# Performance work log

Hardware: AMD Instinct MI355X
Metric: run time of the kernel (lower is better)

The kernel has to match this reference:

```python
import jax, jax.numpy as jnp
import numpy as np

N = 50000   # nodes
E = 500000  # edges
F = 256     # node feature dim
ED = 64     # edge feature dim
H = 128     # hidden channels
O = 32      # out channels
NEG_SLOPE = 0.2
EPS = 1e-16


def setup_inputs() -> dict:
    key = jax.random.key(0)
    ks = jax.random.split(key, 16)
    s = 0.05
    return {
        "x": jax.random.normal(ks[0], (N, F), jnp.float32),
        "edge_index": jax.random.randint(ks[1], (2, E), 0, N, dtype=jnp.int32),
        "edge_attr": jax.random.normal(ks[2], (E, ED), jnp.float32),
        # layer 1 (embed): F -> H
        "W1": jax.random.normal(ks[3], (F, H), jnp.float32) * s,
        "att_src1": jax.random.normal(ks[4], (H,), jnp.float32) * s,
        "att_dst1": jax.random.normal(ks[5], (H,), jnp.float32) * s,
        "We1": jax.random.normal(ks[6], (ED, H), jnp.float32) * s,
        "att_edge1": jax.random.normal(ks[7], (H,), jnp.float32) * s,
        "b1": jnp.zeros((H,), jnp.float32),
        # layer 2 (classifier): H -> O
        "W2": jax.random.normal(ks[8], (H, O), jnp.float32) * s,
        "att_src2": jax.random.normal(ks[9], (O,), jnp.float32) * s,
        "att_dst2": jax.random.normal(ks[10], (O,), jnp.float32) * s,
        "We2": jax.random.normal(ks[11], (ED, O), jnp.float32) * s,
        "att_edge2": jax.random.normal(ks[12], (O,), jnp.float32) * s,
        "b2": jnp.zeros((O,), jnp.float32),
    }


def _add_self_loops_mean(src, dst, ea, n):
    # PyG add_self_loops(fill_value='mean'): self-loop edge_attr = mean of
    # incoming edge_attr per target node (0 for isolated nodes).
    ones = jnp.ones((ea.shape[0],), ea.dtype)
    cnt = jax.ops.segment_sum(ones, dst, num_segments=n)
    summ = jax.ops.segment_sum(ea, dst, num_segments=n)  # [n, ED]
    mean = summ / jnp.maximum(cnt, 1.0)[:, None]
    loop = jnp.arange(n, dtype=src.dtype)
    return (jnp.concatenate([src, loop]),
            jnp.concatenate([dst, loop]),
            jnp.concatenate([ea, mean], axis=0))


def _gat_conv(x, src, dst, ea, W, a_src, a_dst, We, a_edge, b):
    n = x.shape[0]
    src, dst, ea = _add_self_loops_mean(src, dst, ea, n)
    h = x @ W                       # [n, C]
    he = ea @ We                    # [E', C]
    a_s = h @ a_src                 # [n]
    a_d = h @ a_dst                 # [n]
    a_e = he @ a_edge               # [E']
    alpha = a_s[src] + a_d[dst] + a_e
    alpha = jax.nn.leaky_relu(alpha, NEG_SLOPE)
    # segment softmax over incoming edges of each target node
    m = jax.ops.segment_max(alpha, dst, num_segments=n)
    ex = jnp.exp(alpha - m[dst])
    denom = jax.ops.segment_sum(ex, dst, num_segments=n)
    coef = ex / (denom[dst] + EPS)
    out = jax.ops.segment_sum(coef[:, None] * h[src], dst, num_segments=n)
    return out + b


def reference(x, edge_index, edge_attr,
              W1, att_src1, att_dst1, We1, att_edge1, b1,
              W2, att_src2, att_dst2, We2, att_edge2, b2):
    src, dst = edge_index[0], edge_index[1]
    x1 = _gat_conv(x, src, dst, edge_attr, W1, att_src1, att_dst1, We1, att_edge1, b1)
    h = jax.nn.relu(x1)  # Dropout(0.5) is identity in eval mode
    out = _gat_conv(h, src, dst, edge_attr, W2, att_src2, att_dst2, We2, att_edge2, b2)
    return (out, h)
```

## Files before the change

kernel.cpp:

```cpp
#include <hip/hip_runtime.h>

#define N_NODES 50000
#define N_EDGES 500000
#define F_DIM 256
#define ED_DIM 64
#define H_DIM 128
#define O_DIM 32
#define NEG_SLOPE 0.2f
#define EPS_F 1e-16f

#define GB1 391
#define EDGE_BLOCKS 4096

typedef __attribute__((ext_vector_type(8))) short short8;
typedef __attribute__((ext_vector_type(4))) float floatx4;

__device__ __forceinline__ unsigned short f2bf(float f) {
    union { float f; unsigned u; } c; c.f = f;
    unsigned u = c.u;
    return (unsigned short)((u + 0x7fffu + ((u >> 16) & 1u)) >> 16);
}
__device__ __forceinline__ float leaky(float a) { return a > 0.f ? a : a * NEG_SLOPE; }

__global__ void k_prep(const float* __restrict__ We1, const float* __restrict__ aev1,
                       const float* __restrict__ We2, const float* __restrict__ aev2,
                       float* __restrict__ wv1, float* __restrict__ wv2,
                       const float* __restrict__ W1, const float* __restrict__ W2,
                       unsigned short* __restrict__ W1T, unsigned short* __restrict__ W2T) {
    if (blockIdx.x == 32) {
        int t = threadIdx.x;
        if (t < 64) {
            float s = 0.f;
            for (int c = 0; c < H_DIM; c++) s += We1[t * H_DIM + c] * aev1[c];
            wv1[t] = s;
        } else if (t < 128) {
            int k = t - 64;
            float s = 0.f;
            for (int c = 0; c < O_DIM; c++) s += We2[k * O_DIM + c] * aev2[c];
            wv2[k] = s;
        }
        return;
    }
    int gid = blockIdx.x * 256 + threadIdx.x;
    const int stride = 32 * 256;
    for (int i = gid; i < H_DIM * F_DIM; i += stride) {
        int n = i >> 8, k = i & 255;
        W1T[i] = f2bf(W1[k * H_DIM + n]);
    }
    for (int i = gid; i < O_DIM * H_DIM; i += stride) {
        int n = i >> 7, k = i & 127;
        W2T[i] = f2bf(W2[k * O_DIM + n]);
    }
}

__global__ __launch_bounds__(256) void k_fused1(
        const float* __restrict__ A, const unsigned short* __restrict__ BT,
        const float* __restrict__ asv, const float* __restrict__ adv,
        float* __restrict__ C, float* __restrict__ a_s, float* __restrict__ a_d,
        const float* __restrict__ ea, const int* __restrict__ dst,
        const float* __restrict__ wv1, const float* __restrict__ wv2,
        float2* __restrict__ ae12, int* __restrict__ cnt) {
    __shared__ unsigned short As[128 * 40];
    __shared__ unsigned short Bs[128 * 40];
    int tid = threadIdx.x;
    int wave = tid >> 6, lane = tid & 63;

    if (blockIdx.x >= GB1) {
        int bid = blockIdx.x - GB1;
        int sub = lane & 15, eo = lane >> 4;
        float4 w1 = ((const float4*)wv1)[sub];
        float4 w2 = ((const float4*)wv2)[sub];
        int e0 = (bid * 4 + wave) * 4 + eo;
        const int stride = EDGE_BLOCKS * 16;
        for (int e = e0; e < N_EDGES; e += stride) {
            float4 q = *(const float4*)(ea + (size_t)e * ED_DIM + sub * 4);
            float s1 = q.x * w1.x + q.y * w1.y + q.z * w1.z + q.w * w1.w;
            float s2 = q.x * w2.x + q.y * w2.y + q.z * w2.z + q.w * w2.w;
#pragma unroll
            for (int o = 1; o < 16; o <<= 1) {
                s1 += __shfl_xor(s1, o);
                s2 += __shfl_xor(s2, o);
            }
            if (sub == 0) {
                ae12[e] = make_float2(s1, s2);
                atomicAdd(&cnt[dst[e]], 1);
            }
        }
        return;
    }

    int q = lane >> 4, r = lane & 15;
    int bm0 = blockIdx.x * 128;
    floatx4 acc[2][8];
#pragma unroll
    for (int a = 0; a < 2; a++)
#pragma unroll
        for (int b = 0; b < 8; b++) acc[a][b] = (floatx4){0.f, 0.f, 0.f, 0.f};

    int rr = tid >> 3;
    int kc = tid & 7;
    for (int k0 = 0; k0 < 256; k0 += 32) {
#pragma unroll
        for (int i = 0; i < 4; i++) {
            int row = rr + 32 * i;
            int gr = bm0 + row;
            float4 v = make_float4(0.f, 0.f, 0.f, 0.f);
            if (gr < N_NODES) v = *(const float4*)(A + (size_t)gr * 256 + k0 + kc * 4);
            unsigned lo = (unsigned)f2bf(v.x) | ((unsigned)f2bf(v.y) << 16);
            unsigned hi = (unsigned)f2bf(v.z) | ((unsigned)f2bf(v.w) << 16);
            *(uint2*)&As[row * 40 + kc * 4] = make_uint2(lo, hi);
        }
#pragma unroll
        for (int i = 0; i < 2; i++) {
            int idx = tid + 256 * i;
            int n = idx >> 2, ck = idx & 3;
            *(uint4*)&Bs[n * 40 + ck * 8] = *(const uint4*)(BT + n * 256 + k0 + ck * 8);
        }
        __syncthreads();
        short8 af[2], bf[8];
#pragma unroll
        for (int rt = 0; rt < 2; rt++)
            af[rt] = *(const short8*)&As[(wave * 32 + rt * 16 + r) * 40 + q * 8];
#pragma unroll
        for (int nt = 0; nt < 8; nt++)
            bf[nt] = *(const short8*)&Bs[(nt * 16 + r) * 40 + q * 8];
#pragma unroll
        for (int rt = 0; rt < 2; rt++)
#pragma unroll
            for (int nt = 0; nt < 8; nt++)
                acc[rt][nt] = __builtin_amdgcn_mfma_f32_16x16x32_bf16(af[rt], bf[nt], acc[rt][nt], 0, 0, 0);
        __syncthreads();
    }
#pragma unroll
    for (int rt = 0; rt < 2; rt++) {
        int rowb = bm0 + wave * 32 + rt * 16 + q * 4;
        float ps[4] = {0.f, 0.f, 0.f, 0.f}, pd[4] = {0.f, 0.f, 0.f, 0.f};
#pragma unroll
        for (int nt = 0; nt < 8; nt++) {
            int col = nt * 16 + r;
            float av = asv[col], dv = adv[col];
#pragma unroll
            for (int reg = 0; reg < 4; reg++) {
                float v = acc[rt][nt][reg];
                if (rowb + reg < N_NODES) C[(size_t)(rowb + reg) * 128 + col] = v;
                ps[reg] += v * av;
                pd[reg] += v * dv;
            }
        }
#pragma unroll
        for (int reg = 0; reg < 4; reg++) {
#pragma unroll
            for (int off = 1; off < 16; off <<= 1) {
                ps[reg] += __shfl_xor(ps[reg], off);
                pd[reg] += __shfl_xor(pd[reg], off);
            }
        }
        if (r == 0) {
#pragma unroll
            for (int reg = 0; reg < 4; reg++) {
                if (rowb + reg < N_NODES) { a_s[rowb + reg] = ps[reg]; a_d[rowb + reg] = pd[reg]; }
            }
        }
    }
}

__global__ void k_scan1(const int* __restrict__ cnt, int* __restrict__ bsum, int n) {
    __shared__ int sh[256];
    int b = blockIdx.x, t = threadIdx.x;
    int base = b * 1024;
    int s = 0;
    for (int j = 0; j < 4; j++) {
        int idx = base + t * 4 + j;
        if (idx < n) s += cnt[idx];
    }
    sh[t] = s; __syncthreads();
    for (int o = 128; o > 0; o >>= 1) {
        if (t < o) sh[t] += sh[t + o];
        __syncthreads();
    }
    if (t == 0) bsum[b] = sh[0];
}

__global__ void k_scan2(const int* __restrict__ bsum, int* __restrict__ bpre,
                        int* __restrict__ offs, int nb, int n) {
    if (threadIdx.x == 0) {
        int run = 0;
        for (int b = 0; b < nb; b++) { bpre[b] = run; run += bsum[b]; }
        offs[n] = run;
    }
}

__global__ void k_scan3(const int* __restrict__ cnt, const int* __restrict__ bpre,
                        int* __restrict__ offs, int* __restrict__ cursor, int n) {
    __shared__ int sh[256];
    int b = blockIdx.x, t = threadIdx.x;
    int base = b * 1024;
    int v[4]; int s = 0;
    for (int j = 0; j < 4; j++) {
        int idx = base + t * 4 + j;
        v[j] = (idx < n) ? cnt[idx] : 0;
        s += v[j];
    }
    sh[t] = s; __syncthreads();
    for (int o = 1; o < 256; o <<= 1) {
        int x = (t >= o) ? sh[t - o] : 0;
        __syncthreads();
        sh[t] += x;
        __syncthreads();
    }
    int texcl = sh[t] - s + bpre[b];
    int run = 0;
    for (int j = 0; j < 4; j++) {
        int idx = base + t * 4 + j;
        if (idx < n) { offs[idx] = texcl + run; cursor[idx] = texcl + run; }
        run += v[j];
    }
}

__global__ __launch_bounds__(256) void k_scatter(const int* __restrict__ src, const int* __restrict__ dst,
                          const float2* __restrict__ ae12, const float* __restrict__ a_s1,
                          int* __restrict__ cursor, float4* __restrict__ csr) {
    int e = blockIdx.x * blockDim.x + threadIdx.x;
    if (e >= N_EDGES) return;
    int s = src[e];
    int d = dst[e];
    float2 a = ae12[e];
    float as = a_s1[s];
    int p = atomicAdd(&cursor[d], 1);
    csr[p] = make_float4(__int_as_float(s), a.x, a.y, as);
}

template <bool RELU>
__global__ __launch_bounds__(256) void k_agg128(const float* __restrict__ h,
                         const float* __restrict__ a_s, const float* __restrict__ a_d,
                         const int* __restrict__ offs, const float4* __restrict__ csr,
                         const float* __restrict__ bias,
                         float* __restrict__ out) {
    int wave = threadIdx.x >> 6, lane = threadIdx.x & 63;
    int i = blockIdx.x * 4 + wave;
    int r = lane & 15;
    int g = lane >> 4;
    int rs = offs[i], re = offs[i + 1];
    int deg = re - rs;
    float adl = a_d[i];
    float4 acc0 = {0.f, 0.f, 0.f, 0.f}, acc1 = {0.f, 0.f, 0.f, 0.f};
    float dsum = 0.f, sum_ae = 0.f;
    for (int base = rs; base < re; base += 64) {
        int el = base + lane;
        float ex = 0.f, aev = 0.f; int s = 0;
        if (el < re) {
            float4 c = csr[el];
            s = __float_as_int(c.x);
            aev = c.y;
            ex = __expf(leaky(c.w + adl + aev));
        }
        dsum += ex; sum_ae += aev;
        int nv = (re - base) < 64 ? (re - base) : 64;
        int kmax = (nv + 3) >> 2;
        for (int k = 0; k < kmax; k++) {
            int t = g + 4 * k;
            float ext = __shfl(ex, t);
            int st = __shfl(s, t);
            if (t < nv) {
                const float4* hr = (const float4*)(h + (size_t)st * 128);
                float4 v0 = hr[r * 2], v1 = hr[r * 2 + 1];
                acc0.x += ext * v0.x; acc0.y += ext * v0.y; acc0.z += ext * v0.z; acc0.w += ext * v0.w;
                acc1.x += ext * v1.x; acc1.y += ext * v1.y; acc1.z += ext * v1.z; acc1.w += ext * v1.w;
            }
        }
    }
#pragma unroll
    for (int o = 32; o > 0; o >>= 1) {
        dsum += __shfl_xor(dsum, o);
        sum_ae += __shfl_xor(sum_ae, o);
    }
    float loop_ae = sum_ae / (float)(deg > 1 ? deg : 1);
    float al = leaky(a_s[i] + adl + loop_ae);
    float exs = __expf(al);
    float* a0 = (float*)&acc0; float* a1 = (float*)&acc1;
#pragma unroll
    for (int c = 0; c < 4; c++) {
        a0[c] += __shfl_xor(a0[c], 16); a0[c] += __shfl_xor(a0[c], 32);
        a1[c] += __shfl_xor(a1[c], 16); a1[c] += __shfl_xor(a1[c], 32);
    }
    if (g == 0) {
        float inv = 1.0f / (dsum + exs + EPS_F);
        const float4* hr = (const float4*)(h + (size_t)i * 128);
        float4 h0 = hr[r * 2], h1 = hr[r * 2 + 1];
        const float4* bp = (const float4*)bias;
        float4 b0 = bp[r * 2], b1 = bp[r * 2 + 1];
        float4 o0, o1;
        o0.x = (a0[0] + exs * h0.x) * inv + b0.x;
        o0.y = (a0[1] + exs * h0.y) * inv + b0.y;
        o0.z = (a0[2] + exs * h0.z) * inv + b0.z;
        o0.w = (a0[3] + exs * h0.w) * inv + b0.w;
        o1.x = (a1[0] + exs * h1.x) * inv + b1.x;
        o1.y = (a1[1] + exs * h1.y) * inv + b1.y;
        o1.z = (a1[2] + exs * h1.z) * inv + b1.z;
        o1.w = (a1[3] + exs * h1.w) * inv + b1.w;
        if (RELU) {
            o0.x = fmaxf(o0.x, 0.f); o0.y = fmaxf(o0.y, 0.f); o0.z = fmaxf(o0.z, 0.f); o0.w = fmaxf(o0.w, 0.f);
            o1.x = fmaxf(o1.x, 0.f); o1.y = fmaxf(o1.y, 0.f); o1.z = fmaxf(o1.z, 0.f); o1.w = fmaxf(o1.w, 0.f);
        }
        float4* op = (float4*)(out + (size_t)i * 128);
        op[r * 2] = o0;
        op[r * 2 + 1] = o1;
    }
}

__global__ __launch_bounds__(256) void k_gemm2(const float* __restrict__ A,
        const unsigned short* __restrict__ BT,
        const float* __restrict__ asv, const float* __restrict__ adv,
        float* __restrict__ C, float* __restrict__ a_s, float* __restrict__ a_d, int M) {
    __shared__ unsigned short As[128 * 40];
    __shared__ unsigned short Bs[32 * 40];
    int tid = threadIdx.x;
    int wave = tid >> 6, lane = tid & 63;
    int q = lane >> 4, r = lane & 15;
    int bm0 = blockIdx.x * 128;
    floatx4 acc[2][2];
#pragma unroll
    for (int a = 0; a < 2; a++)
#pragma unroll
        for (int b = 0; b < 2; b++) acc[a][b] = (floatx4){0.f, 0.f, 0.f, 0.f};

    int rr = tid >> 3;
    int kc = tid & 7;
    for (int k0 = 0; k0 < 128; k0 += 32) {
#pragma unroll
        for (int i = 0; i < 4; i++) {
            int row = rr + 32 * i;
            int gr = bm0 + row;
            float4 v = make_float4(0.f, 0.f, 0.f, 0.f);
            if (gr < M) v = *(const float4*)(A + (size_t)gr * 128 + k0 + kc * 4);
            unsigned lo = (unsigned)f2bf(v.x) | ((unsigned)f2bf(v.y) << 16);
            unsigned hi = (unsigned)f2bf(v.z) | ((unsigned)f2bf(v.w) << 16);
            *(uint2*)&As[row * 40 + kc * 4] = make_uint2(lo, hi);
        }
        if (tid < 128) {
            int n = tid >> 2, ck = tid & 3;
            *(uint4*)&Bs[n * 40 + ck * 8] = *(const uint4*)(BT + n * 128 + k0 + ck * 8);
        }
        __syncthreads();
        short8 af[2], bf[2];
#pragma unroll
        for (int rt = 0; rt < 2; rt++)
            af[rt] = *(const short8*)&As[(wave * 32 + rt * 16 + r) * 40 + q * 8];
#pragma unroll
        for (int nt = 0; nt < 2; nt++)
            bf[nt] = *(const short8*)&Bs[(nt * 16 + r) * 40 + q * 8];
#pragma unroll
        for (int rt = 0; rt < 2; rt++)
#pragma unroll
            for (int nt = 0; nt < 2; nt++)
                acc[rt][nt] = __builtin_amdgcn_mfma_f32_16x16x32_bf16(af[rt], bf[nt], acc[rt][nt], 0, 0, 0);
        __syncthreads();
    }
#pragma unroll
    for (int rt = 0; rt < 2; rt++) {
        int rowb = bm0 + wave * 32 + rt * 16 + q * 4;
        float ps[4] = {0.f, 0.f, 0.f, 0.f}, pd[4] = {0.f, 0.f, 0.f, 0.f};
#pragma unroll
        for (int nt = 0; nt < 2; nt++) {
            int col = nt * 16 + r;
            float av = asv[col], dv = adv[col];
#pragma unroll
            for (int reg = 0; reg < 4; reg++) {
                float v = acc[rt][nt][reg];
                if (rowb + reg < M) C[(size_t)(rowb + reg) * 32 + col] = v;
                ps[reg] += v * av;
                pd[reg] += v * dv;
            }
        }
#pragma unroll
        for (int reg = 0; reg < 4; reg++) {
#pragma unroll
            for (int off = 1; off < 16; off <<= 1) {
                ps[reg] += __shfl_xor(ps[reg], off);
                pd[reg] += __shfl_xor(pd[reg], off);
            }
        }
        if (r == 0) {
#pragma unroll
            for (int reg = 0; reg < 4; reg++) {
                if (rowb + reg < M) { a_s[rowb + reg] = ps[reg]; a_d[rowb + reg] = pd[reg]; }
            }
        }
    }
}

__global__ __launch_bounds__(256) void k_agg32(const float* __restrict__ h,
                        const float* __restrict__ a_s, const float* __restrict__ a_d,
                        const int* __restrict__ offs, const float4* __restrict__ csr,
                        const float* __restrict__ bias,
                        float* __restrict__ out) {
    int wave = threadIdx.x >> 6, lane = threadIdx.x & 63;
    int i = blockIdx.x * 4 + wave;
    int r = lane & 7;
    int g = lane >> 3;
    int rs = offs[i], re = offs[i + 1];
    int deg = re - rs;
    float adl = a_d[i];
    float4 acc = {0.f, 0.f, 0.f, 0.f};
    float dsum = 0.f, sum_ae = 0.f;
    for (int base = rs; base < re; base += 64) {
        int el = base + lane;
        float ex = 0.f, aev = 0.f; int s = 0;
        if (el < re) {
            float4 c = csr[el];
            s = __float_as_int(c.x);
            aev = c.z;
            ex = __expf(leaky(a_s[s] + adl + aev));
        }
        dsum += ex; sum_ae += aev;
        int nv = (re - base) < 64 ? (re - base) : 64;
        int kmax = (nv + 7) >> 3;
        for (int k = 0; k < kmax; k++) {
            int t = g + 8 * k;
            float ext = __shfl(ex, t);
            int st = __shfl(s, t);
            if (t < nv) {
                float4 v = ((const float4*)(h + (size_t)st * 32))[r];
                acc.x += ext * v.x; acc.y += ext * v.y; acc.z += ext * v.z; acc.w += ext * v.w;
            }
        }
    }
#pragma unroll
    for (int o = 32; o > 0; o >>= 1) {
        dsum += __shfl_xor(dsum, o);
        sum_ae += __shfl_xor(sum_ae, o);
    }
    float loop_ae = sum_ae / (float)(deg > 1 ? deg : 1);
    float al = leaky(a_s[i] + adl + loop_ae);
    float exs = __expf(al);
#pragma unroll
    for (int o = 8; o < 64; o <<= 1) {
        acc.x += __shfl_xor(acc.x, o); acc.y += __shfl_xor(acc.y, o);
        acc.z += __shfl_xor(acc.z, o); acc.w += __shfl_xor(acc.w, o);
    }
    if (g == 0) {
        float inv = 1.0f / (dsum + exs + EPS_F);
        float4 hv = ((const float4*)(h + (size_t)i * 32))[r];
        float4 bv = ((const float4*)bias)[r];
        float4 ov;
        ov.x = (acc.x + exs * hv.x) * inv + bv.x;
        ov.y = (acc.y + exs * hv.y) * inv + bv.y;
        ov.z = (acc.z + exs * hv.z) * inv + bv.z;
        ov.w = (acc.w + exs * hv.w) * inv + bv.w;
        ((float4*)(out + (size_t)i * 32))[r] = ov;
    }
}

extern "C" void kernel_launch(void* const* d_in, const int* in_sizes, int n_in,
                              void* d_out, int out_size, void* d_ws, size_t ws_size,
                              hipStream_t stream) {
    const float* x    = (const float*)d_in[0];
    const int* ei     = (const int*)d_in[1];
    const float* ea   = (const float*)d_in[2];
    const float* W1   = (const float*)d_in[3];
    const float* as1v = (const float*)d_in[4];
    const float* ad1v = (const float*)d_in[5];
    const float* We1  = (const float*)d_in[6];
    const float* aev1 = (const float*)d_in[7];
    const float* b1   = (const float*)d_in[8];
    const float* W2   = (const float*)d_in[9];
    const float* as2v = (const float*)d_in[10];
    const float* ad2v = (const float*)d_in[11];
    const float* We2  = (const float*)d_in[12];
    const float* aev2 = (const float*)d_in[13];
    const float* b2   = (const float*)d_in[14];

    const int* src = ei;
    const int* dst = ei + N_EDGES;

    char* w = (char*)d_ws;
    size_t off = 0;
    auto alloc = [&](size_t bytes) -> void* {
        void* p = w + off;
        off += bytes;
        off = (off + 255) & ~(size_t)255;
        return p;
    };
    float* h1      = (float*)alloc((size_t)N_NODES * H_DIM * 4);
    float* h2      = (float*)alloc((size_t)N_NODES * O_DIM * 4);
    float2* ae12   = (float2*)alloc((size_t)N_EDGES * 8);
    int* cnt       = (int*)alloc((size_t)N_NODES * 4);
    int* offs      = (int*)alloc((size_t)(N_NODES + 1) * 4);
    int* cursor    = (int*)alloc((size_t)N_NODES * 4);
    float4* csr    = (float4*)alloc((size_t)N_EDGES * 16);
    int* bsum      = (int*)alloc(64 * 4);
    int* bpre      = (int*)alloc(64 * 4);
    float* wv1     = (float*)alloc(64 * 4);
    float* wv2     = (float*)alloc(64 * 4);
    float* a_s1    = (float*)alloc((size_t)N_NODES * 4);
    float* a_d1    = (float*)alloc((size_t)N_NODES * 4);
    float* a_s2    = (float*)alloc((size_t)N_NODES * 4);
    float* a_d2    = (float*)alloc((size_t)N_NODES * 4);
    unsigned short* W1T = (unsigned short*)alloc((size_t)H_DIM * F_DIM * 2);
    unsigned short* W2T = (unsigned short*)alloc((size_t)O_DIM * H_DIM * 2);

    hipMemsetAsync(cnt, 0, (size_t)N_NODES * 4, stream);

    k_prep<<<33, 256, 0, stream>>>(We1, aev1, We2, aev2, wv1, wv2, W1, W2, W1T, W2T);

    k_fused1<<<GB1 + EDGE_BLOCKS, 256, 0, stream>>>(x, W1T, as1v, ad1v,
                                                    h1, a_s1, a_d1,
                                                    ea, dst, wv1, wv2, ae12, cnt);

    int nb = (N_NODES + 1023) / 1024;
    k_scan1<<<nb, 256, 0, stream>>>(cnt, bsum, N_NODES);
    k_scan2<<<1, 64, 0, stream>>>(bsum, bpre, offs, nb, N_NODES);
    k_scan3<<<nb, 256, 0, stream>>>(cnt, bpre, offs, cursor, N_NODES);

    k_scatter<<<(N_EDGES + 255) / 256, 256, 0, stream>>>(src, dst, ae12, a_s1,
                                                         cursor, csr);

    float* out = (float*)d_out;
    float* h_out = out + (size_t)N_NODES * O_DIM;

    k_agg128<true><<<(N_NODES + 3) / 4, 256, 0, stream>>>(h1, a_s1, a_d1, offs,
                                                          csr, b1, h_out);

    k_gemm2<<<(N_NODES + 127) / 128, 256, 0, stream>>>(h_out, W2T, as2v, ad2v,
                                                       h2, a_s2, a_d2, N_NODES);
    k_agg32<<<(N_NODES + 3) / 4, 256, 0, stream>>>(h2, a_s2, a_d2, offs,
                                                   csr, b2, out);
}
```

Baseline: 406.7 us.

## Split fused GEMM/edge kernel, fold layer-2 attention into agg128, prefetch shuffles

Splits the combined GEMM1 plus edge-attention kernel into two separate launches, and the edge kernel now has each lane handle 16 floats of an edge row with fewer shuffles. The hipMemset of the degree counts moves into the prep kernel. Layer-2 source/destination attention scores are computed in agg128 from W2·att vectors precomputed in prep, so gemm2 no longer reduces them. The agg kernels prefetch the next neighbour's index and weight shuffles, a software-pipelining step. The aim is fewer launches, a leaner gemm2 and better latency hiding, at the cost of losing overlap between GEMM1 and the edge pass and adding a small fp32 rounding difference in the layer-2 scores.

```diff
diff --git a/kernel.cpp b/kernel.cpp
--- a/kernel.cpp
+++ b/kernel.cpp
@@ -9,8 +9,7 @@
 #define NEG_SLOPE 0.2f
 #define EPS_F 1e-16f
 
-#define GB1 391
-#define EDGE_BLOCKS 4096
+#define EB 2048
 
 typedef __attribute__((ext_vector_type(8))) short short8;
 typedef __attribute__((ext_vector_type(4))) float floatx4;
@@ -21,12 +20,18 @@
     return (unsigned short)((u + 0x7fffu + ((u >> 16) & 1u)) >> 16);
 }
 __device__ __forceinline__ float leaky(float a) { return a > 0.f ? a : a * NEG_SLOPE; }
+__device__ __forceinline__ float dot4(float4 a, float4 b) {
+    return a.x * b.x + a.y * b.y + a.z * b.z + a.w * b.w;
+}
 
 __global__ void k_prep(const float* __restrict__ We1, const float* __restrict__ aev1,
                        const float* __restrict__ We2, const float* __restrict__ aev2,
                        float* __restrict__ wv1, float* __restrict__ wv2,
                        const float* __restrict__ W1, const float* __restrict__ W2,
-                       unsigned short* __restrict__ W1T, unsigned short* __restrict__ W2T) {
+                       const float* __restrict__ as2v, const float* __restrict__ ad2v,
+                       float* __restrict__ was2, float* __restrict__ wad2,
+                       unsigned short* __restrict__ W1T, unsigned short* __restrict__ W2T,
+                       int* __restrict__ cnt) {
     if (blockIdx.x == 32) {
         int t = threadIdx.x;
         if (t < 64) {
@@ -38,11 +43,21 @@
             float s = 0.f;
             for (int c = 0; c < O_DIM; c++) s += We2[k * O_DIM + c] * aev2[c];
             wv2[k] = s;
+        } else {
+            int c = t - 128;
+            float s = 0.f, d = 0.f;
+            for (int o = 0; o < O_DIM; o++) {
+                float w = W2[c * O_DIM + o];
+                s += w * as2v[o];
+                d += w * ad2v[o];
+            }
+            was2[c] = s; wad2[c] = d;
         }
         return;
     }
     int gid = blockIdx.x * 256 + threadIdx.x;
     const int stride = 32 * 256;
+    for (int i = gid; i < N_NODES; i += stride) cnt[i] = 0;
     for (int i = gid; i < H_DIM * F_DIM; i += stride) {
         int n = i >> 8, k = i & 255;
         W1T[i] = f2bf(W1[k * H_DIM + n]);
@@ -53,42 +68,43 @@
     }
 }
 
-__global__ __launch_bounds__(256) void k_fused1(
-        const float* __restrict__ A, const unsigned short* __restrict__ BT,
-        const float* __restrict__ asv, const float* __restrict__ adv,
-        float* __restrict__ C, float* __restrict__ a_s, float* __restrict__ a_d,
+__global__ __launch_bounds__(256) void k_edge_ae(
         const float* __restrict__ ea, const int* __restrict__ dst,
         const float* __restrict__ wv1, const float* __restrict__ wv2,
         float2* __restrict__ ae12, int* __restrict__ cnt) {
+    int tid = threadIdx.x;
+    int wave = tid >> 6, lane = tid & 63;
+    int sub = lane & 3, eg = lane >> 2;
+    float4 w1[4], w2[4];
+#pragma unroll
+    for (int j = 0; j < 4; j++) {
+        w1[j] = ((const float4*)wv1)[sub * 4 + j];
+        w2[j] = ((const float4*)wv2)[sub * 4 + j];
+    }
+    int g0 = (blockIdx.x * 4 + wave) * 16 + eg;
+    const int stride = EB * 64;
+    for (int e = g0; e < N_EDGES; e += stride) {
+        const float4* row = (const float4*)(ea + (size_t)e * ED_DIM + sub * 16);
+        float4 q0 = row[0], q1 = row[1], q2 = row[2], q3 = row[3];
+        float s1 = dot4(q0, w1[0]) + dot4(q1, w1[1]) + dot4(q2, w1[2]) + dot4(q3, w1[3]);
+        float s2 = dot4(q0, w2[0]) + dot4(q1, w2[1]) + dot4(q2, w2[2]) + dot4(q3, w2[3]);
+        s1 += __shfl_xor(s1, 1); s2 += __shfl_xor(s2, 1);
+        s1 += __shfl_xor(s1, 2); s2 += __shfl_xor(s2, 2);
+        if (sub == 0) {
+            ae12[e] = make_float2(s1, s2);
+            atomicAdd(&cnt[dst[e]], 1);
+        }
+    }
+}
+
+__global__ __launch_bounds__(256) void k_gemm1(const float* __restrict__ A,
+        const unsigned short* __restrict__ BT,
+        const float* __restrict__ asv, const float* __restrict__ adv,
+        float* __restrict__ C, float* __restrict__ a_s, float* __restrict__ a_d, int M) {
     __shared__ unsigned short As[128 * 40];
     __shared__ unsigned short Bs[128 * 40];
     int tid = threadIdx.x;
     int wave = tid >> 6, lane = tid & 63;
-
-    if (blockIdx.x >= GB1) {
-        int bid = blockIdx.x - GB1;
-        int sub = lane & 15, eo = lane >> 4;
-        float4 w1 = ((const float4*)wv1)[sub];
-        float4 w2 = ((const float4*)wv2)[sub];
-        int e0 = (bid * 4 + wave) * 4 + eo;
-        const int stride = EDGE_BLOCKS * 16;
-        for (int e = e0; e < N_EDGES; e += stride) {
-            float4 q = *(const float4*)(ea + (size_t)e * ED_DIM + sub * 4);
-            float s1 = q.x * w1.x + q.y * w1.y + q.z * w1.z + q.w * w1.w;
-            float s2 = q.x * w2.x + q.y * w2.y + q.z * w2.z + q.w * w2.w;
-#pragma unroll
-            for (int o = 1; o < 16; o <<= 1) {
-                s1 += __shfl_xor(s1, o);
-                s2 += __shfl_xor(s2, o);
-            }
-            if (sub == 0) {
-                ae12[e] = make_float2(s1, s2);
-                atomicAdd(&cnt[dst[e]], 1);
-            }
-        }
-        return;
-    }
-
     int q = lane >> 4, r = lane & 15;
     int bm0 = blockIdx.x * 128;
     floatx4 acc[2][8];
@@ -105,7 +121,7 @@
             int row = rr + 32 * i;
             int gr = bm0 + row;
             float4 v = make_float4(0.f, 0.f, 0.f, 0.f);
-            if (gr < N_NODES) v = *(const float4*)(A + (size_t)gr * 256 + k0 + kc * 4);
+            if (gr < M) v = *(const float4*)(A + (size_t)gr * 256 + k0 + kc * 4);
             unsigned lo = (unsigned)f2bf(v.x) | ((unsigned)f2bf(v.y) << 16);
             unsigned hi = (unsigned)f2bf(v.z) | ((unsigned)f2bf(v.w) << 16);
             *(uint2*)&As[row * 40 + kc * 4] = make_uint2(lo, hi);
@@ -142,7 +158,7 @@
 #pragma unroll
             for (int reg = 0; reg < 4; reg++) {
                 float v = acc[rt][nt][reg];
-                if (rowb + reg < N_NODES) C[(size_t)(rowb + reg) * 128 + col] = v;
+                if (rowb + reg < M) C[(size_t)(rowb + reg) * 128 + col] = v;
                 ps[reg] += v * av;
                 pd[reg] += v * dv;
             }
@@ -158,7 +174,7 @@
         if (r == 0) {
 #pragma unroll
             for (int reg = 0; reg < 4; reg++) {
-                if (rowb + reg < N_NODES) { a_s[rowb + reg] = ps[reg]; a_d[rowb + reg] = pd[reg]; }
+                if (rowb + reg < M) { a_s[rowb + reg] = ps[reg]; a_d[rowb + reg] = pd[reg]; }
             }
         }
     }
@@ -235,6 +251,8 @@
                          const float* __restrict__ a_s, const float* __restrict__ a_d,
                          const int* __restrict__ offs, const float4* __restrict__ csr,
                          const float* __restrict__ bias,
+                         const float* __restrict__ was2, const float* __restrict__ wad2,
+                         float* __restrict__ a_s2, float* __restrict__ a_d2,
                          float* __restrict__ out) {
     int wave = threadIdx.x >> 6, lane = threadIdx.x & 63;
     int i = blockIdx.x * 4 + wave;
@@ -257,16 +275,20 @@
         dsum += ex; sum_ae += aev;
         int nv = (re - base) < 64 ? (re - base) : 64;
         int kmax = (nv + 3) >> 2;
+        float ext = __shfl(ex, g);
+        int st = __shfl(s, g);
         for (int k = 0; k < kmax; k++) {
+            int tn = (g + 4 * (k + 1)) & 63;
+            float extn = __shfl(ex, tn);
+            int stn = __shfl(s, tn);
             int t = g + 4 * k;
-            float ext = __shfl(ex, t);
-            int st = __shfl(s, t);
             if (t < nv) {
                 const float4* hr = (const float4*)(h + (size_t)st * 128);
                 float4 v0 = hr[r * 2], v1 = hr[r * 2 + 1];
                 acc0.x += ext * v0.x; acc0.y += ext * v0.y; acc0.z += ext * v0.z; acc0.w += ext * v0.w;
                 acc1.x += ext * v1.x; acc1.y += ext * v1.y; acc1.z += ext * v1.z; acc1.w += ext * v1.w;
             }
+            ext = extn; st = stn;
         }
     }
 #pragma unroll
@@ -305,13 +327,22 @@
         float4* op = (float4*)(out + (size_t)i * 128);
         op[r * 2] = o0;
         op[r * 2 + 1] = o1;
+        float4 wsa = ((const float4*)was2)[r * 2], wsb = ((const float4*)was2)[r * 2 + 1];
+        float4 wda = ((const float4*)wad2)[r * 2], wdb = ((const float4*)wad2)[r * 2 + 1];
+        float ps = dot4(o0, wsa) + dot4(o1, wsb);
+        float pd = dot4(o0, wda) + dot4(o1, wdb);
+#pragma unroll
+        for (int o = 1; o < 16; o <<= 1) {
+            ps += __shfl_xor(ps, o);
+            pd += __shfl_xor(pd, o);
+        }
+        if (r == 0) { a_s2[i] = ps; a_d2[i] = pd; }
     }
 }
 
 __global__ __launch_bounds__(256) void k_gemm2(const float* __restrict__ A,
         const unsigned short* __restrict__ BT,
-        const float* __restrict__ asv, const float* __restrict__ adv,
-        float* __restrict__ C, float* __restrict__ a_s, float* __restrict__ a_d, int M) {
+        float* __restrict__ C, int M) {
     __shared__ unsigned short As[128 * 40];
     __shared__ unsigned short Bs[32 * 40];
     int tid = threadIdx.x;
@@ -359,31 +390,12 @@
 #pragma unroll
     for (int rt = 0; rt < 2; rt++) {
         int rowb = bm0 + wave * 32 + rt * 16 + q * 4;
-        float ps[4] = {0.f, 0.f, 0.f, 0.f}, pd[4] = {0.f, 0.f, 0.f, 0.f};
 #pragma unroll
         for (int nt = 0; nt < 2; nt++) {
             int col = nt * 16 + r;
-            float av = asv[col], dv = adv[col];
 #pragma unroll
             for (int reg = 0; reg < 4; reg++) {
-                float v = acc[rt][nt][reg];
-                if (rowb + reg < M) C[(size_t)(rowb + reg) * 32 + col] = v;
-                ps[reg] += v * av;
-                pd[reg] += v * dv;
-            }
-        }
-#pragma unroll
-        for (int reg = 0; reg < 4; reg++) {
-#pragma unroll
-            for (int off = 1; off < 16; off <<= 1) {
-                ps[reg] += __shfl_xor(ps[reg], off);
-                pd[reg] += __shfl_xor(pd[reg], off);
-            }
-        }
-        if (r == 0) {
-#pragma unroll
-            for (int reg = 0; reg < 4; reg++) {
-                if (rowb + reg < M) { a_s[rowb + reg] = ps[reg]; a_d[rowb + reg] = pd[reg]; }
+                if (rowb + reg < M) C[(size_t)(rowb + reg) * 32 + col] = acc[rt][nt][reg];
             }
         }
     }
@@ -415,14 +427,18 @@
         dsum += ex; sum_ae += aev;
         int nv = (re - base) < 64 ? (re - base) : 64;
         int kmax = (nv + 7) >> 3;
+        float ext = __shfl(ex, g);
+        int st = __shfl(s, g);
         for (int k = 0; k < kmax; k++) {
+            int tn = (g + 8 * (k + 1)) & 63;
+            float extn = __shfl(ex, tn);
+            int stn = __shfl(s, tn);
             int t = g + 8 * k;
-            float ext = __shfl(ex, t);
-            int st = __shfl(s, t);
             if (t < nv) {
                 float4 v = ((const float4*)(h + (size_t)st * 32))[r];
                 acc.x += ext * v.x; acc.y += ext * v.y; acc.z += ext * v.z; acc.w += ext * v.w;
             }
+            ext = extn; st = stn;
         }
     }
 #pragma unroll
@@ -492,6 +508,8 @@
     int* bpre      = (int*)alloc(64 * 4);
     float* wv1     = (float*)alloc(64 * 4);
     float* wv2     = (float*)alloc(64 * 4);
+    float* was2    = (float*)alloc(128 * 4);
+    float* wad2    = (float*)alloc(128 * 4);
     float* a_s1    = (float*)alloc((size_t)N_NODES * 4);
     float* a_d1    = (float*)alloc((size_t)N_NODES * 4);
     float* a_s2    = (float*)alloc((size_t)N_NODES * 4);
@@ -499,13 +517,13 @@
     unsigned short* W1T = (unsigned short*)alloc((size_t)H_DIM * F_DIM * 2);
     unsigned short* W2T = (unsigned short*)alloc((size_t)O_DIM * H_DIM * 2);
 
-    hipMemsetAsync(cnt, 0, (size_t)N_NODES * 4, stream);
-
-    k_prep<<<33, 256, 0, stream>>>(We1, aev1, We2, aev2, wv1, wv2, W1, W2, W1T, W2T);
-
-    k_fused1<<<GB1 + EDGE_BLOCKS, 256, 0, stream>>>(x, W1T, as1v, ad1v,
-                                                    h1, a_s1, a_d1,
-                                                    ea, dst, wv1, wv2, ae12, cnt);
+    k_prep<<<33, 256, 0, stream>>>(We1, aev1, We2, aev2, wv1, wv2, W1, W2,
+                                   as2v, ad2v, was2, wad2, W1T, W2T, cnt);
+
+    k_edge_ae<<<EB, 256, 0, stream>>>(ea, dst, wv1, wv2, ae12, cnt);
+
+    k_gemm1<<<(N_NODES + 127) / 128, 256, 0, stream>>>(x, W1T, as1v, ad1v,
+                                                       h1, a_s1, a_d1, N_NODES);
 
     int nb = (N_NODES + 1023) / 1024;
     k_scan1<<<nb, 256, 0, stream>>>(cnt, bsum, N_NODES);
@@ -519,10 +537,11 @@
     float* h_out = out + (size_t)N_NODES * O_DIM;
 
     k_agg128<true><<<(N_NODES + 3) / 4, 256, 0, stream>>>(h1, a_s1, a_d1, offs,
-                                                          csr, b1, h_out);
-
-    k_gemm2<<<(N_NODES + 127) / 128, 256, 0, stream>>>(h_out, W2T, as2v, ad2v,
-                                                       h2, a_s2, a_d2, N_NODES);
+                                                          csr, b1, was2, wad2,
+                                                          a_s2, a_d2, h_out);
+
+    k_gemm2<<<(N_NODES + 127) / 128, 256, 0, stream>>>(h_out, W2T, h2, N_NODES);
+
     k_agg32<<<(N_NODES + 3) / 4, 256, 0, stream>>>(h2, a_s2, a_d2, offs,
                                                    csr, b2, out);
 }
```

New measurement: 390.0 us. 1.04x faster.
